# Kernel optimization log

Measured on AMD Instinct MI355X. Metric: run time of the kernel, lower is better.

The kernel has to match this reference:

```python
import jax, jax.numpy as jnp
import numpy as np

N = 20000   # nodes
E = 320000  # edges
L = 16      # text length per node
T = 64      # num_text_features
H = 128     # num_hidden_features
V = 32000   # vocab_size
NS = 2      # num_samples
C = 2       # num_classes
F = 8       # num_node_features


def setup_inputs() -> dict:
    key = jax.random.key(0)
    ks = jax.random.split(key, 20)
    def rn(k, shape, scale=0.05):
        return jax.random.normal(k, shape, jnp.float32) * scale
    return {
        "x": jax.random.normal(ks[0], (N, F), jnp.float32),
        "edge_index": jax.random.randint(ks[1], (2, E), 0, N),
        "xtext": jax.random.randint(ks[2], (N, L), 0, V),
        "image_features": jax.random.normal(ks[3], (N, H * NS), jnp.float32),
        "conv1_w": rn(ks[4], (F, H)), "conv1_b": jnp.zeros((H,), jnp.float32),
        "conv2_w": rn(ks[5], (H, H)), "conv2_b": jnp.zeros((H,), jnp.float32),
        "embed": rn(ks[6], (V, T), 1.0),
        "gru_wih": rn(ks[7], (3 * H, T)), "gru_whh": rn(ks[8], (3 * H, H)),
        "gru_bih": jnp.zeros((3 * H,), jnp.float32), "gru_bhh": jnp.zeros((3 * H,), jnp.float32),
        "lin_pos_w": rn(ks[9], (2 * H, H)), "lin_pos_b": jnp.zeros((H,), jnp.float32),
        "lin_text_w": rn(ks[10], (2 * H, H)), "lin_text_b": jnp.zeros((H,), jnp.float32),
        "lin_img_w": rn(ks[11], (2 * H * NS, H)), "lin_img_b": jnp.zeros((H,), jnp.float32),
        "row_w1": rn(ks[12], (3 * H, H)), "row_b1": jnp.zeros((H,), jnp.float32),
        "row_w2": rn(ks[13], (H, C)), "row_b2": jnp.zeros((C,), jnp.float32),
        "col_w1": rn(ks[14], (3 * H, H)), "col_b1": jnp.zeros((H,), jnp.float32),
        "col_w2": rn(ks[15], (H, C)), "col_b2": jnp.zeros((C,), jnp.float32),
    }


def gcn(x, w, b, src, dst, n):
    xw = x @ w  # [N, H]
    deg = jnp.zeros((n,), xw.dtype).at[dst].add(1.0) + 1.0
    dinv = jax.lax.rsqrt(deg)
    norm = dinv[src] * dinv[dst]  # [E]
    agg = jax.ops.segment_sum(xw[src] * norm[:, None], dst, num_segments=n)
    agg = agg + xw * (dinv * dinv)[:, None]  # self-loop term
    return agg + b


def gru_sum(x_seq, wih, whh, bih, bhh):
    # x_seq: [N, L, T]; torch GRU cell; return sum over time of outputs -> [N, H]
    h0 = jnp.zeros((x_seq.shape[0], whh.shape[1]), x_seq.dtype)
    def step(h, xt):
        gi = xt @ wih.T + bih
        gh = h @ whh.T + bhh
        ir, iz, inn = jnp.split(gi, 3, axis=-1)
        hr, hz, hn = jnp.split(gh, 3, axis=-1)
        r = jax.nn.sigmoid(ir + hr)
        z = jax.nn.sigmoid(iz + hz)
        nn_ = jnp.tanh(inn + r * hn)
        h2 = (1.0 - z) * nn_ + z * h
        return h2, h2
    _, ys = jax.lax.scan(step, h0, jnp.swapaxes(x_seq, 0, 1))  # ys: [L, N, H]
    return jnp.sum(ys, axis=0)


def reference(x, edge_index, xtext, image_features,
              conv1_w, conv1_b, conv2_w, conv2_b, embed,
              gru_wih, gru_whh, gru_bih, gru_bhh,
              lin_pos_w, lin_pos_b, lin_text_w, lin_text_b, lin_img_w, lin_img_b,
              row_w1, row_b1, row_w2, row_b2, col_w1, col_b1, col_w2, col_b2):
    src, dst = edge_index[0], edge_index[1]
    n = x.shape[0]
    h1 = jax.nn.relu(gcn(x, conv1_w, conv1_b, src, dst, n))
    pos = jax.nn.relu(gcn(h1, conv2_w, conv2_b, src, dst, n))
    txt = gru_sum(embed[xtext], gru_wih, gru_whh, gru_bih, gru_bhh)

    def edge_feat(feat, w, b):
        cat = jnp.concatenate([feat[src], feat[dst]], axis=1)
        return jax.nn.relu(cat @ w + b)

    ep = edge_feat(pos, lin_pos_w, lin_pos_b)
    et = edge_feat(txt, lin_text_w, lin_text_b)
    ei = edge_feat(image_features, lin_img_w, lin_img_b)
    e = jnp.concatenate([ep, et, ei], axis=1)  # [E, 3H]
    row_pred = jax.nn.log_softmax(jax.nn.relu(e @ row_w1 + row_b1) @ row_w2 + row_b2, axis=1)
    col_pred = jax.nn.log_softmax(jax.nn.relu(e @ col_w1 + col_b1) @ col_w2 + col_b2, axis=1)
    return (row_pred, col_pred)
```

## Files before the change

kernel.cpp:

```cpp
#include <hip/hip_runtime.h>
#include <hip/hip_bf16.h>

#define NN 20000
#define NE 320000
#define LL 16
#define TT 64
#define HH 128

typedef __attribute__((ext_vector_type(8))) short short8v;
typedef __attribute__((ext_vector_type(4))) float f32x4;
#define MFMA_BF16(a,b,c) __builtin_amdgcn_mfma_f32_16x16x32_bf16(a,b,c,0,0,0)

__device__ inline unsigned short f32_to_bf16(float v) {
  unsigned int b = __float_as_uint(v);
  b += 0x7fffu + ((b >> 16) & 1u);
  return (unsigned short)(b >> 16);
}
__device__ inline float bf16_to_f32(unsigned short u) {
  return __uint_as_float(((unsigned int)u) << 16);
}
__device__ inline float fast_sigmoid(float x) {
  return __builtin_amdgcn_rcpf(1.f + __expf(-x));
}
__device__ inline float fast_tanh(float x) {
  float e = __expf(2.f * x);
  return 1.f - 2.f * __builtin_amdgcn_rcpf(e + 1.f);
}
__device__ inline unsigned int cvt_pk_bf16(float lo, float hi) {
  unsigned int r;
  asm("v_cvt_pk_bf16_f32 %0, %1, %2" : "=v"(r) : "v"(lo), "v"(hi));
  return r;
}
__device__ inline unsigned int combine2(unsigned int us, unsigned int ud) {
  float sl = __uint_as_float(us << 16);
  float sh = __uint_as_float(us & 0xffff0000u);
  float dl = __uint_as_float(ud << 16);
  float dh = __uint_as_float(ud & 0xffff0000u);
  return cvt_pk_bf16(fmaxf(sl + dl, 0.f), fmaxf(sh + dh, 0.f));
}

__global__ void prep_k(
    const float* __restrict__ gwih, const float* __restrict__ gwhh,
    const float* __restrict__ rw1, const float* __restrict__ cw1,
    const float* __restrict__ conv2w,
    const float* __restrict__ lpw, const float* __restrict__ ltw, const float* __restrict__ liw,
    const float* __restrict__ lpb, const float* __restrict__ ltb, const float* __restrict__ lib,
    const float* __restrict__ gbih, const float* __restrict__ gbhh,
    unsigned short* __restrict__ wihB, unsigned short* __restrict__ whhB,
    unsigned short* __restrict__ rw1T, unsigned short* __restrict__ cw1T,
    unsigned short* __restrict__ conv2T,
    unsigned short* __restrict__ TposW, unsigned short* __restrict__ TtxtW,
    unsigned short* __restrict__ TimgW,
    float* __restrict__ bcomb, float* __restrict__ brz,
    float* __restrict__ binv, float* __restrict__ bhnv)
{
  int i = blockIdx.x * 256 + threadIdx.x;
  if (i < 24576) { wihB[i] = f32_to_bf16(gwih[i]); return; } i -= 24576;
  if (i < 49152) { whhB[i] = f32_to_bf16(gwhh[i]); return; } i -= 49152;
  if (i < 49152) { int c = i / 384, r = i - c * 384; rw1T[i] = f32_to_bf16(rw1[r * 128 + c]); return; } i -= 49152;
  if (i < 49152) { int c = i / 384, r = i - c * 384; cw1T[i] = f32_to_bf16(cw1[r * 128 + c]); return; } i -= 49152;
  if (i < 16384) { int c = i / 128, r = i - c * 128; conv2T[i] = f32_to_bf16(conv2w[r * 128 + c]); return; } i -= 16384;
  if (i < 32768) { int col = i / 128, k = i - col * 128;
    float v = (col < 128) ? lpw[k * 128 + col] : lpw[(128 + k) * 128 + (col - 128)];
    TposW[i] = f32_to_bf16(v); return; } i -= 32768;
  if (i < 32768) { int col = i / 128, k = i - col * 128;
    float v = (col < 128) ? ltw[k * 128 + col] : ltw[(128 + k) * 128 + (col - 128)];
    TtxtW[i] = f32_to_bf16(v); return; } i -= 32768;
  if (i < 65536) { int col = i / 256, k = i - col * 256;
    float v = (col < 128) ? liw[k * 128 + col] : liw[(256 + k) * 128 + (col - 128)];
    TimgW[i] = f32_to_bf16(v); return; } i -= 65536;
  if (i < 768) { int t = i >> 8, j = i & 255;
    const float* b = t == 0 ? lpb : t == 1 ? ltb : lib;
    bcomb[i] = (j < 128) ? 0.f : b[j - 128]; return; } i -= 768;
  if (i < 512) {
    if (i < 256) brz[i] = gbih[i] + gbhh[i];
    else if (i < 384) binv[i - 256] = gbih[i];
    else bhnv[i - 384] = gbhh[i - 128];
  }
}

__global__ void cvtf2_k(const float* __restrict__ in, unsigned int* __restrict__ out, int n2) {
  int i = blockIdx.x * 256 + threadIdx.x;
  if (i < n2) {
    float2 v = reinterpret_cast<const float2*>(in)[i];
    out[i] = cvt_pk_bf16(v.x, v.y);
  }
}

__global__ void fill_zero_k(float* __restrict__ p, int n) {
  int i = blockIdx.x * 256 + threadIdx.x;
  if (i < n) p[i] = 0.f;
}

__global__ void histo_k(const int* __restrict__ eidx, int* __restrict__ ideg) {
  int e = blockIdx.x * 256 + threadIdx.x;
  if (e < NE) atomicAdd(&ideg[eidx[NE + e]], 1);
}

__global__ void scan_k(const int* __restrict__ ideg, int* __restrict__ rowptr) {
  __shared__ int sh[256];
  __shared__ int carry;
  const int tid = threadIdx.x;
  if (tid == 0) carry = 0;
  __syncthreads();
  for (int base = 0; base < NN; base += 256) {
    int v = (base + tid < NN) ? ideg[base + tid] : 0;
    sh[tid] = v;
    __syncthreads();
#pragma unroll
    for (int off = 1; off < 256; off <<= 1) {
      int t = (tid >= off) ? sh[tid - off] : 0;
      __syncthreads();
      sh[tid] += t;
      __syncthreads();
    }
    if (base + tid < NN) rowptr[base + tid] = carry + sh[tid] - v;
    __syncthreads();
    if (tid == 255) carry += sh[255];
    __syncthreads();
  }
  if (tid == 0) rowptr[NN] = carry;
}

__global__ void dinv_csr_k(const int* __restrict__ rowptr, float* __restrict__ dinv) {
  int i = blockIdx.x * 256 + threadIdx.x;
  if (i < NN) dinv[i] = rsqrtf((float)(rowptr[i + 1] - rowptr[i]) + 1.f);
}

__global__ void scatter_k(const int* __restrict__ eidx, int* __restrict__ cursor,
                          int* __restrict__ esrc_s, int* __restrict__ edst_s,
                          int* __restrict__ eorig_s) {
  int e = blockIdx.x * 256 + threadIdx.x;
  if (e >= NE) return;
  int s = eidx[e], d = eidx[NE + e];
  int pos = atomicAdd(&cursor[d], 1);
  esrc_s[pos] = s;
  edst_s[pos] = d;
  eorig_s[pos] = e;
}

__global__ void xw1_k(const float* __restrict__ x, const float* __restrict__ w,
                      const float* __restrict__ dinv, unsigned int* __restrict__ xws) {
  int i = blockIdx.x * 256 + threadIdx.x;
  if (i >= NN * 64) return;
  int n = i >> 6, c2 = (i & 63) * 2;
  float a0 = 0.f, a1 = 0.f;
#pragma unroll
  for (int k = 0; k < 8; ++k) {
    float xv = x[n * 8 + k];
    a0 += xv * w[k * 128 + c2];
    a1 += xv * w[k * 128 + c2 + 1];
  }
  float dn = dinv[n];
  xws[i] = cvt_pk_bf16(a0 * dn, a1 * dn);
}

__global__ __launch_bounds__(256) void gcn_csr_k(
    const int* __restrict__ rowptr, const int* __restrict__ esrc_s,
    const unsigned int* __restrict__ xws, const float* __restrict__ dinv,
    const float* __restrict__ bias, unsigned int* __restrict__ outB)
{
  int node = blockIdx.x * 4 + (threadIdx.x >> 6);
  int lane = threadIdx.x & 63;
  if (node >= NN) return;
  float dd = dinv[node];
  int beg = rowptr[node], end = rowptr[node + 1];
  float a0 = 0.f, a1 = 0.f;
  int i = beg;
  for (; i + 1 < end; i += 2) {
    int s0 = esrc_s[i], s1 = esrc_s[i + 1];
    unsigned int u0 = xws[s0 * 64 + lane];
    unsigned int u1 = xws[s1 * 64 + lane];
    a0 += __uint_as_float(u0 << 16) + __uint_as_float(u1 << 16);
    a1 += __uint_as_float(u0 & 0xffff0000u) + __uint_as_float(u1 & 0xffff0000u);
  }
  if (i < end) {
    unsigned int u = xws[esrc_s[i] * 64 + lane];
    a0 += __uint_as_float(u << 16);
    a1 += __uint_as_float(u & 0xffff0000u);
  }
  unsigned int un = xws[node * 64 + lane];
  a0 += __uint_as_float(un << 16);
  a1 += __uint_as_float(un & 0xffff0000u);
  a0 = fmaxf(a0 * dd + bias[lane * 2], 0.f);
  a1 = fmaxf(a1 * dd + bias[lane * 2 + 1], 0.f);
  outB[node * 64 + lane] = cvt_pk_bf16(a0, a1);
}

template<int KDIM, int NCOLS, bool OUTBF16, bool ADDBIAS, bool SCALEROW>
__global__ __launch_bounds__(256) void gemm_mfma_k(
    const unsigned short* __restrict__ A, const unsigned short* __restrict__ WT,
    const float* __restrict__ bias, const float* __restrict__ rowscale,
    void* __restrict__ Cv, int M)
{
  const int tid = threadIdx.x;
  const int wid = tid >> 6, lane = tid & 63;
  const int l16 = lane & 15, lk = lane >> 4;
  const int bm = blockIdx.x * 128, bn = blockIdx.y * 128;
  const int wr = wid * 32;

  int row[2];
#pragma unroll
  for (int mf = 0; mf < 2; ++mf) {
    int r = bm + wr + mf * 16 + l16;
    row[mf] = r < M ? r : M - 1;
  }
  f32x4 acc[2][8];
#pragma unroll
  for (int mf = 0; mf < 2; ++mf)
#pragma unroll
    for (int nf = 0; nf < 8; ++nf) acc[mf][nf] = f32x4{0.f, 0.f, 0.f, 0.f};

#pragma unroll
  for (int kc = 0; kc < KDIM / 32; ++kc) {
    short8v a[2];
#pragma unroll
    for (int mf = 0; mf < 2; ++mf)
      a[mf] = *reinterpret_cast<const short8v*>(&A[(size_t)row[mf] * KDIM + kc * 32 + lk * 8]);
#pragma unroll
    for (int nf = 0; nf < 8; ++nf) {
      int col = bn + nf * 16 + l16;
      short8v b = *reinterpret_cast<const short8v*>(&WT[(size_t)col * KDIM + kc * 32 + lk * 8]);
      acc[0][nf] = MFMA_BF16(a[0], b, acc[0][nf]);
      acc[1][nf] = MFMA_BF16(a[1], b, acc[1][nf]);
    }
  }
#pragma unroll
  for (int mf = 0; mf < 2; ++mf)
#pragma unroll
    for (int nf = 0; nf < 8; ++nf) {
      int col = bn + nf * 16 + l16;
      float bb = ADDBIAS ? bias[col] : 0.f;
#pragma unroll
      for (int reg = 0; reg < 4; ++reg) {
        int r = bm + wr + mf * 16 + lk * 4 + reg;
        if (r < M) {
          float v = acc[mf][nf][reg] + bb;
          if (SCALEROW) v *= rowscale[r];
          if (OUTBF16) ((unsigned short*)Cv)[(size_t)r * NCOLS + col] = f32_to_bf16(v);
          else         ((float*)Cv)[(size_t)r * NCOLS + col] = v;
        }
      }
    }
}

__global__ __launch_bounds__(256, 2) void gru_fused_k(
    const int* __restrict__ xtext, const float* __restrict__ embed,
    const unsigned short* __restrict__ wihB, const unsigned short* __restrict__ whhB,
    const float* __restrict__ brz, const float* __restrict__ binv, const float* __restrict__ bhnv,
    unsigned short* __restrict__ txt)
{
  __shared__ unsigned char hs[2][32 * 256];
  __shared__ unsigned char xs[32 * 128];
  const int tid = threadIdx.x;
  const int n0 = blockIdx.x * 32;
  const int wid = tid >> 6, lane = tid & 63;
  const int l16 = lane & 15, lk = lane >> 4;

  for (int i = tid; i < 32 * 256 / 4; i += 256) ((unsigned int*)hs[0])[i] = 0u;

  short8v wR[2][2], wZ[2][2], wN[2][2];
  short8v uR[2][4], uZ[2][4], uN[2][4];
  float bRr[2], bZr[2], bIr[2], bHr[2];
#pragma unroll
  for (int cf = 0; cf < 2; ++cf) {
    int col = wid * 32 + cf * 16 + l16;
#pragma unroll
    for (int ks = 0; ks < 2; ++ks) {
      wR[cf][ks] = *reinterpret_cast<const short8v*>(&wihB[(col      ) * 64 + ks * 32 + lk * 8]);
      wZ[cf][ks] = *reinterpret_cast<const short8v*>(&wihB[(col + 128) * 64 + ks * 32 + lk * 8]);
      wN[cf][ks] = *reinterpret_cast<const short8v*>(&wihB[(col + 256) * 64 + ks * 32 + lk * 8]);
    }
#pragma unroll
    for (int ks = 0; ks < 4; ++ks) {
      uR[cf][ks] = *reinterpret_cast<const short8v*>(&whhB[(col      ) * 128 + ks * 32 + lk * 8]);
      uZ[cf][ks] = *reinterpret_cast<const short8v*>(&whhB[(col + 128) * 128 + ks * 32 + lk * 8]);
      uN[cf][ks] = *reinterpret_cast<const short8v*>(&whhB[(col + 256) * 128 + ks * 32 + lk * 8]);
    }
    bRr[cf] = brz[col]; bZr[cf] = brz[128 + col];
    bIr[cf] = binv[col]; bHr[cf] = bhnv[col];
  }

  f32x4 txtacc[2][2];
#pragma unroll
  for (int mf = 0; mf < 2; ++mf)
#pragma unroll
    for (int cf = 0; cf < 2; ++cf) txtacc[mf][cf] = f32x4{0.f, 0.f, 0.f, 0.f};

  int cur = 0;
  for (int t = 0; t < LL; ++t) {
    __syncthreads();
    {
      const int k4 = tid & 15, r0 = tid >> 4;
#pragma unroll
      for (int rep = 0; rep < 2; ++rep) {
        int row = r0 + rep * 16;
        int n = n0 + row; if (n >= NN) n = NN - 1;
        int tok = xtext[n * LL + t];
        float4 v = *reinterpret_cast<const float4*>(&embed[(size_t)tok * TT + k4 * 4]);
        ushort4 w;
        w.x = f32_to_bf16(v.x); w.y = f32_to_bf16(v.y);
        w.z = f32_to_bf16(v.z); w.w = f32_to_bf16(v.w);
        *reinterpret_cast<ushort4*>(&xs[row * 128 + ((k4 * 8) ^ ((row & 7) << 4))]) = w;
      }
    }
    __syncthreads();

#pragma unroll
    for (int mf = 0; mf < 2; ++mf) {
      const int arow = mf * 16 + l16;
      const int asw = (arow & 7) << 4;
      short8v ax[2], ah[4];
#pragma unroll
      for (int ks = 0; ks < 2; ++ks)
        ax[ks] = *reinterpret_cast<const short8v*>(&xs[arow * 128 + ((ks * 64 + lk * 16) ^ asw)]);
#pragma unroll
      for (int ks = 0; ks < 4; ++ks)
        ah[ks] = *reinterpret_cast<const short8v*>(&hs[cur][arow * 256 + ((ks * 64 + lk * 16) ^ asw)]);

      f32x4 aR[2], aZ[2], aI[2], aHn[2];
#pragma unroll
      for (int cf = 0; cf < 2; ++cf) {
        aR[cf] = f32x4{0.f, 0.f, 0.f, 0.f}; aZ[cf] = f32x4{0.f, 0.f, 0.f, 0.f};
        aI[cf] = f32x4{0.f, 0.f, 0.f, 0.f}; aHn[cf] = f32x4{0.f, 0.f, 0.f, 0.f};
#pragma unroll
        for (int ks = 0; ks < 2; ++ks) {
          aR[cf] = MFMA_BF16(ax[ks], wR[cf][ks], aR[cf]);
          aZ[cf] = MFMA_BF16(ax[ks], wZ[cf][ks], aZ[cf]);
          aI[cf] = MFMA_BF16(ax[ks], wN[cf][ks], aI[cf]);
        }
#pragma unroll
        for (int ks = 0; ks < 4; ++ks) {
          aR[cf]  = MFMA_BF16(ah[ks], uR[cf][ks], aR[cf]);
          aZ[cf]  = MFMA_BF16(ah[ks], uZ[cf][ks], aZ[cf]);
          aHn[cf] = MFMA_BF16(ah[ks], uN[cf][ks], aHn[cf]);
        }
      }

#pragma unroll
      for (int cf = 0; cf < 2; ++cf) {
        const int j = wid * 32 + cf * 16 + l16;
#pragma unroll
        for (int reg = 0; reg < 4; ++reg) {
          const int row = mf * 16 + lk * 4 + reg;
          const int byte = row * 256 + ((j * 2) ^ ((row & 7) << 4));
          float hold = bf16_to_f32(*reinterpret_cast<unsigned short*>(&hs[cur][byte]));
          float rg = fast_sigmoid(aR[cf][reg] + bRr[cf]);
          float zg = fast_sigmoid(aZ[cf][reg] + bZr[cf]);
          float ng = fast_tanh(aI[cf][reg] + bIr[cf] + rg * (aHn[cf][reg] + bHr[cf]));
          float h2 = (1.f - zg) * ng + zg * hold;
          txtacc[mf][cf][reg] += h2;
          *reinterpret_cast<unsigned short*>(&hs[cur ^ 1][byte]) = f32_to_bf16(h2);
        }
      }
    }
    cur ^= 1;
  }

#pragma unroll
  for (int mf = 0; mf < 2; ++mf)
#pragma unroll
    for (int cf = 0; cf < 2; ++cf) {
      const int j = wid * 32 + cf * 16 + l16;
#pragma unroll
      for (int reg = 0; reg < 4; ++reg) {
        const int row = mf * 16 + lk * 4 + reg;
        const int n = n0 + row;
        if (n < NN) txt[(size_t)n * HH + j] = f32_to_bf16(txtacc[mf][cf][reg]);
      }
    }
}

__global__ __launch_bounds__(256, 2) void edge_mfma_k(
    const int* __restrict__ esrc_s, const int* __restrict__ edst_s,
    const int* __restrict__ eorig_s,
    const unsigned short* __restrict__ Tall,
    const unsigned short* __restrict__ rw1T, const float* __restrict__ rb1,
    const float* __restrict__ rw2, const float* __restrict__ rb2,
    const unsigned short* __restrict__ cw1T, const float* __restrict__ cb1,
    const float* __restrict__ cw2, const float* __restrict__ cb2,
    float* __restrict__ out)
{
  const int tid = threadIdx.x;
  const int e0 = blockIdx.x * 128;
  const int wid = tid >> 6, lane = tid & 63;
  const int l16 = lane & 15, lk = lane >> 4;
  const int wr = wid * 32;
  const int lkoff = lk * 8;

  const int ea = e0 + wr + l16, eb = e0 + wr + 16 + l16;
  const size_t soff0 = (size_t)esrc_s[ea] * 256;
  const size_t soff1 = (size_t)esrc_s[eb] * 256;
  const size_t doff0 = (size_t)edst_s[ea] * 256 + 128;
  const size_t doff1 = (size_t)edst_s[eb] * 256 + 128;

  uint4 af[6][2][2];
  uint4 dr[2][2][2];
  f32x4 acc[2][8];
#pragma unroll
  for (int mf = 0; mf < 2; ++mf)
#pragma unroll
    for (int nf = 0; nf < 8; ++nf) acc[mf][nf] = f32x4{0.f, 0.f, 0.f, 0.f};

#define TB(c) (Tall + (size_t)((c) >> 1) * ((size_t)NN * 256) + ((c) & 1) * 64 + lkoff)
#define LSRC(c) { const unsigned short* tb = TB(c); \
  af[c][0][0] = *reinterpret_cast<const uint4*>(tb + soff0); \
  af[c][0][1] = *reinterpret_cast<const uint4*>(tb + soff0 + 32); \
  af[c][1][0] = *reinterpret_cast<const uint4*>(tb + soff1); \
  af[c][1][1] = *reinterpret_cast<const uint4*>(tb + soff1 + 32); }
#define LDST(c) { const unsigned short* tb = TB(c); \
  dr[(c) & 1][0][0] = *reinterpret_cast<const uint4*>(tb + doff0); \
  dr[(c) & 1][0][1] = *reinterpret_cast<const uint4*>(tb + doff0 + 32); \
  dr[(c) & 1][1][0] = *reinterpret_cast<const uint4*>(tb + doff1); \
  dr[(c) & 1][1][1] = *reinterpret_cast<const uint4*>(tb + doff1 + 32); }
#define COMB(c) { \
  _Pragma("unroll") for (int mf = 0; mf < 2; ++mf) \
  _Pragma("unroll") for (int ks = 0; ks < 2; ++ks) { \
    uint4 s = af[c][mf][ks], d = dr[(c) & 1][mf][ks]; \
    uint4 r; r.x = combine2(s.x, d.x); r.y = combine2(s.y, d.y); \
    r.z = combine2(s.z, d.z); r.w = combine2(s.w, d.w); \
    af[c][mf][ks] = r; } }
#define PROCH(c, W) { \
  _Pragma("unroll") for (int ks = 0; ks < 2; ++ks) { \
    short8v a0 = *reinterpret_cast<short8v*>(&af[c][0][ks]); \
    short8v a1 = *reinterpret_cast<short8v*>(&af[c][1][ks]); \
    int kglob = (c) * 64 + ks * 32 + lkoff; \
    _Pragma("unroll") for (int nf = 0; nf < 8; ++nf) { \
      int col = nf * 16 + l16; \
      short8v b = *reinterpret_cast<const short8v*>(&W[(size_t)col * 384 + kglob]); \
      acc[0][nf] = MFMA_BF16(a0, b, acc[0][nf]); \
      acc[1][nf] = MFMA_BF16(a1, b, acc[1][nf]); } } }
#define EPI(B1, W2, B2, H) { \
  _Pragma("unroll") for (int mf = 0; mf < 2; ++mf) \
  _Pragma("unroll") for (int reg = 0; reg < 4; ++reg) { \
    float p0 = 0.f, p1 = 0.f; \
    _Pragma("unroll") for (int nf = 0; nf < 8; ++nf) { \
      int col = nf * 16 + l16; \
      float hv = fmaxf(acc[mf][nf][reg] + B1[col], 0.f); \
      p0 += hv * W2[col * 2]; p1 += hv * W2[col * 2 + 1]; } \
    _Pragma("unroll") for (int m = 1; m < 16; m <<= 1) { \
      p0 += __shfl_xor(p0, m); p1 += __shfl_xor(p1, m); } \
    if (l16 == 0) { \
      int orig = eorig_s[e0 + wr + mf * 16 + lk * 4 + reg]; \
      float l0 = p0 + B2[0], l1 = p1 + B2[1]; \
      float mx = fmaxf(l0, l1); \
      float lse = mx + __logf(__expf(l0 - mx) + __expf(l1 - mx)); \
      float2 o2 = make_float2(l0 - lse, l1 - lse); \
      *reinterpret_cast<float2*>(&out[(size_t)(H) * 2 * NE + (size_t)orig * 2]) = o2; } } }

  LSRC(0) LSRC(1) LSRC(2) LSRC(3) LSRC(4) LSRC(5)
  LDST(0) LDST(1)
  COMB(0) PROCH(0, rw1T) LDST(2)
  COMB(1) PROCH(1, rw1T) LDST(3)
  COMB(2) PROCH(2, rw1T) LDST(4)
  COMB(3) PROCH(3, rw1T) LDST(5)
  COMB(4) PROCH(4, rw1T)
  COMB(5) PROCH(5, rw1T)
  EPI(rb1, rw2, rb2, 0)

#pragma unroll
  for (int mf = 0; mf < 2; ++mf)
#pragma unroll
    for (int nf = 0; nf < 8; ++nf) acc[mf][nf] = f32x4{0.f, 0.f, 0.f, 0.f};

  __builtin_amdgcn_s_setprio(1);
  PROCH(0, cw1T) PROCH(1, cw1T) PROCH(2, cw1T)
  PROCH(3, cw1T) PROCH(4, cw1T) PROCH(5, cw1T)
  __builtin_amdgcn_s_setprio(0);
  EPI(cb1, cw2, cb2, 1)

#undef TB
#undef LSRC
#undef LDST
#undef COMB
#undef PROCH
#undef EPI
}

extern "C" void kernel_launch(void* const* d_in, const int* in_sizes, int n_in,
                              void* d_out, int out_size, void* d_ws, size_t ws_size,
                              hipStream_t stream)
{
  const float* x       = (const float*)d_in[0];
  const int*   eidx    = (const int*)  d_in[1];
  const int*   xtext   = (const int*)  d_in[2];
  const float* imgf    = (const float*)d_in[3];
  const float* conv1_w = (const float*)d_in[4];
  const float* conv1_b = (const float*)d_in[5];
  const float* conv2_w = (const float*)d_in[6];
  const float* conv2_b = (const float*)d_in[7];
  const float* embed   = (const float*)d_in[8];
  const float* gwih    = (const float*)d_in[9];
  const float* gwhh    = (const float*)d_in[10];
  const float* gbih    = (const float*)d_in[11];
  const float* gbhh    = (const float*)d_in[12];
  const float* lpw     = (const float*)d_in[13];
  const float* lpb     = (const float*)d_in[14];
  const float* ltw     = (const float*)d_in[15];
  const float* ltb     = (const float*)d_in[16];
  const float* liw     = (const float*)d_in[17];
  const float* lib     = (const float*)d_in[18];
  const float* rw1     = (const float*)d_in[19];
  const float* rb1     = (const float*)d_in[20];
  const float* rw2     = (const float*)d_in[21];
  const float* rb2     = (const float*)d_in[22];
  const float* cw1     = (const float*)d_in[23];
  const float* cb1     = (const float*)d_in[24];
  const float* cw2     = (const float*)d_in[25];
  const float* cb2     = (const float*)d_in[26];
  float* out = (float*)d_out;

  char* w8 = (char*)d_ws;
  size_t off = 0;
  auto balloc = [&](size_t bytes) { void* p = w8 + off; off = (off + bytes + 255) & ~(size_t)255; return p; };
  float*          dinv   = (float*)balloc(NN * 4);
  int*            ideg   = (int*)balloc((NN + 1) * 4);
  int*            rowptr = (int*)balloc((NN + 1) * 4);
  int*            cursor = (int*)balloc((NN + 1) * 4);
  int*            esrc_s = (int*)balloc((size_t)NE * 4);
  int*            edst_s = (int*)balloc((size_t)NE * 4);
  int*            eorig_s= (int*)balloc((size_t)NE * 4);
  unsigned int*   xwsB   = (unsigned int*)balloc((size_t)NN * 64 * 4);
  unsigned int*   nodeB  = (unsigned int*)balloc((size_t)NN * 64 * 4);
  unsigned short* txtB   = (unsigned short*)balloc((size_t)NN * HH * 2);
  unsigned short* imgB   = (unsigned short*)balloc((size_t)NN * 256 * 2);
  unsigned short* Tall   = (unsigned short*)balloc((size_t)3 * NN * 256 * 2);
  unsigned short* wihB   = (unsigned short*)balloc(384 * 64 * 2);
  unsigned short* whhB   = (unsigned short*)balloc(384 * 128 * 2);
  unsigned short* rw1T   = (unsigned short*)balloc(384 * 128 * 2);
  unsigned short* cw1T   = (unsigned short*)balloc(384 * 128 * 2);
  unsigned short* conv2T = (unsigned short*)balloc(128 * 128 * 2);
  unsigned short* TposW  = (unsigned short*)balloc(256 * 128 * 2);
  unsigned short* TtxtW  = (unsigned short*)balloc(256 * 128 * 2);
  unsigned short* TimgW  = (unsigned short*)balloc(256 * 256 * 2);
  float*          bcomb  = (float*)balloc(768 * 4);
  float*          brz    = (float*)balloc(256 * 4);
  float*          binv   = (float*)balloc(128 * 4);
  float*          bhnv   = (float*)balloc(128 * 4);

  dim3 b256(256);
  auto cdiv = [](int a, int b) { return (a + b - 1) / b; };
  const int MB = cdiv(NN, 128);

  prep_k<<<cdiv(320768, 256), b256, 0, stream>>>(
      gwih, gwhh, rw1, cw1, conv2_w, lpw, ltw, liw, lpb, ltb, lib, gbih, gbhh,
      wihB, whhB, rw1T, cw1T, conv2T, TposW, TtxtW, TimgW, bcomb, brz, binv, bhnv);
  cvtf2_k<<<cdiv(NN * 128, 256), b256, 0, stream>>>(imgf, (unsigned int*)imgB, NN * 128);

  fill_zero_k<<<cdiv(NN + 1, 256), b256, 0, stream>>>((float*)ideg, NN + 1);
  histo_k<<<cdiv(NE, 256), b256, 0, stream>>>(eidx, ideg);
  scan_k<<<1, b256, 0, stream>>>(ideg, rowptr);
  dinv_csr_k<<<cdiv(NN, 256), b256, 0, stream>>>(rowptr, dinv);
  hipMemcpyAsync(cursor, rowptr, (NN + 1) * sizeof(int), hipMemcpyDeviceToDevice, stream);
  scatter_k<<<cdiv(NE, 256), b256, 0, stream>>>(eidx, cursor, esrc_s, edst_s, eorig_s);

  xw1_k<<<cdiv(NN * 64, 256), b256, 0, stream>>>(x, conv1_w, dinv, xwsB);
  gcn_csr_k<<<cdiv(NN, 4), b256, 0, stream>>>(rowptr, esrc_s, xwsB, dinv, conv1_b, nodeB);

  gemm_mfma_k<128, 128, true, false, true><<<dim3(MB, 1), b256, 0, stream>>>(
      (const unsigned short*)nodeB, conv2T, nullptr, dinv, xwsB, NN);
  gcn_csr_k<<<cdiv(NN, 4), b256, 0, stream>>>(rowptr, esrc_s, xwsB, dinv, conv2_b, nodeB);

  gru_fused_k<<<NN / 32, b256, 0, stream>>>(xtext, embed, wihB, whhB, brz, binv, bhnv, txtB);

  gemm_mfma_k<128, 256, true, true, false><<<dim3(MB, 2), b256, 0, stream>>>(
      (const unsigned short*)nodeB, TposW, bcomb, nullptr, Tall, NN);
  gemm_mfma_k<128, 256, true, true, false><<<dim3(MB, 2), b256, 0, stream>>>(
      txtB, TtxtW, bcomb + 256, nullptr, Tall + (size_t)NN * 256, NN);
  gemm_mfma_k<256, 256, true, true, false><<<dim3(MB, 2), b256, 0, stream>>>(
      imgB, TimgW, bcomb + 512, nullptr, Tall + (size_t)2 * NN * 256, NN);

  edge_mfma_k<<<NE / 128, b256, 0, stream>>>(esrc_s, edst_s, eorig_s, Tall,
                                             rw1T, rb1, rw2, rb2, cw1T, cb1, cw2, cb2, out);
}
```

Before: 795.6 us.

## Restructure edge kernel to 16 edges per wave with fused row/col heads

The edge MLP kernel now gives each wave 16 edges instead of 32 and computes the row and column hidden layers together in one pass over K. The A fragment is built once per K-slice and fed to both weight matrices, so the 6-chunk register cache of gathered features is no longer needed. Launch bounds rise to 4 blocks per SM and the grid doubles. The intent is lower register pressure and higher occupancy to hide gather latency. The cost is that each weight fragment load now serves half as many MFMAs, which increases weight traffic per edge.

Measured after the change: 998.7 us. +25.5%, slower.

```diff
diff --git a/kernel.cpp b/kernel.cpp
--- a/kernel.cpp
+++ b/kernel.cpp
@@ -371,7 +371,7 @@
     }
 }
 
-__global__ __launch_bounds__(256, 2) void edge_mfma_k(
+__global__ __launch_bounds__(256, 4) void edge_mfma_k(
     const int* __restrict__ esrc_s, const int* __restrict__ edst_s,
     const int* __restrict__ eorig_s,
     const unsigned short* __restrict__ Tall,
@@ -382,99 +382,89 @@
     float* __restrict__ out)
 {
   const int tid = threadIdx.x;
-  const int e0 = blockIdx.x * 128;
   const int wid = tid >> 6, lane = tid & 63;
   const int l16 = lane & 15, lk = lane >> 4;
-  const int wr = wid * 32;
+  const int e0 = blockIdx.x * 64 + wid * 16;
   const int lkoff = lk * 8;
 
-  const int ea = e0 + wr + l16, eb = e0 + wr + 16 + l16;
-  const size_t soff0 = (size_t)esrc_s[ea] * 256;
-  const size_t soff1 = (size_t)esrc_s[eb] * 256;
-  const size_t doff0 = (size_t)edst_s[ea] * 256 + 128;
-  const size_t doff1 = (size_t)edst_s[eb] * 256 + 128;
-
-  uint4 af[6][2][2];
-  uint4 dr[2][2][2];
-  f32x4 acc[2][8];
-#pragma unroll
-  for (int mf = 0; mf < 2; ++mf)
-#pragma unroll
-    for (int nf = 0; nf < 8; ++nf) acc[mf][nf] = f32x4{0.f, 0.f, 0.f, 0.f};
+  const size_t soff = (size_t)esrc_s[e0 + l16] * 256;
+  const size_t doff = (size_t)edst_s[e0 + l16] * 256 + 128;
+
+  f32x4 acc0[8], acc1[8];
+#pragma unroll
+  for (int nf = 0; nf < 8; ++nf) {
+    acc0[nf] = f32x4{0.f, 0.f, 0.f, 0.f};
+    acc1[nf] = f32x4{0.f, 0.f, 0.f, 0.f};
+  }
+
+  uint4 sr[2][2], dr[2][2];
 
 #define TB(c) (Tall + (size_t)((c) >> 1) * ((size_t)NN * 256) + ((c) & 1) * 64 + lkoff)
-#define LSRC(c) { const unsigned short* tb = TB(c); \
-  af[c][0][0] = *reinterpret_cast<const uint4*>(tb + soff0); \
-  af[c][0][1] = *reinterpret_cast<const uint4*>(tb + soff0 + 32); \
-  af[c][1][0] = *reinterpret_cast<const uint4*>(tb + soff1); \
-  af[c][1][1] = *reinterpret_cast<const uint4*>(tb + soff1 + 32); }
-#define LDST(c) { const unsigned short* tb = TB(c); \
-  dr[(c) & 1][0][0] = *reinterpret_cast<const uint4*>(tb + doff0); \
-  dr[(c) & 1][0][1] = *reinterpret_cast<const uint4*>(tb + doff0 + 32); \
-  dr[(c) & 1][1][0] = *reinterpret_cast<const uint4*>(tb + doff1); \
-  dr[(c) & 1][1][1] = *reinterpret_cast<const uint4*>(tb + doff1 + 32); }
-#define COMB(c) { \
-  _Pragma("unroll") for (int mf = 0; mf < 2; ++mf) \
+#define LD(c) { const unsigned short* tb = TB(c); \
+  sr[(c) & 1][0] = *reinterpret_cast<const uint4*>(tb + soff); \
+  sr[(c) & 1][1] = *reinterpret_cast<const uint4*>(tb + soff + 32); \
+  dr[(c) & 1][0] = *reinterpret_cast<const uint4*>(tb + doff); \
+  dr[(c) & 1][1] = *reinterpret_cast<const uint4*>(tb + doff + 32); }
+#define PROC(c) { \
   _Pragma("unroll") for (int ks = 0; ks < 2; ++ks) { \
-    uint4 s = af[c][mf][ks], d = dr[(c) & 1][mf][ks]; \
-    uint4 r; r.x = combine2(s.x, d.x); r.y = combine2(s.y, d.y); \
-    r.z = combine2(s.z, d.z); r.w = combine2(s.w, d.w); \
-    af[c][mf][ks] = r; } }
-#define PROCH(c, W) { \
-  _Pragma("unroll") for (int ks = 0; ks < 2; ++ks) { \
-    short8v a0 = *reinterpret_cast<short8v*>(&af[c][0][ks]); \
-    short8v a1 = *reinterpret_cast<short8v*>(&af[c][1][ks]); \
+    uint4 s = sr[(c) & 1][ks], d = dr[(c) & 1][ks]; \
+    unsigned int afr[4]; \
+    afr[0] = combine2(s.x, d.x); afr[1] = combine2(s.y, d.y); \
+    afr[2] = combine2(s.z, d.z); afr[3] = combine2(s.w, d.w); \
+    short8v a = *reinterpret_cast<short8v*>(afr); \
     int kglob = (c) * 64 + ks * 32 + lkoff; \
     _Pragma("unroll") for (int nf = 0; nf < 8; ++nf) { \
       int col = nf * 16 + l16; \
-      short8v b = *reinterpret_cast<const short8v*>(&W[(size_t)col * 384 + kglob]); \
-      acc[0][nf] = MFMA_BF16(a0, b, acc[0][nf]); \
-      acc[1][nf] = MFMA_BF16(a1, b, acc[1][nf]); } } }
-#define EPI(B1, W2, B2, H) { \
-  _Pragma("unroll") for (int mf = 0; mf < 2; ++mf) \
-  _Pragma("unroll") for (int reg = 0; reg < 4; ++reg) { \
-    float p0 = 0.f, p1 = 0.f; \
-    _Pragma("unroll") for (int nf = 0; nf < 8; ++nf) { \
-      int col = nf * 16 + l16; \
-      float hv = fmaxf(acc[mf][nf][reg] + B1[col], 0.f); \
-      p0 += hv * W2[col * 2]; p1 += hv * W2[col * 2 + 1]; } \
-    _Pragma("unroll") for (int m = 1; m < 16; m <<= 1) { \
-      p0 += __shfl_xor(p0, m); p1 += __shfl_xor(p1, m); } \
-    if (l16 == 0) { \
-      int orig = eorig_s[e0 + wr + mf * 16 + lk * 4 + reg]; \
-      float l0 = p0 + B2[0], l1 = p1 + B2[1]; \
-      float mx = fmaxf(l0, l1); \
-      float lse = mx + __logf(__expf(l0 - mx) + __expf(l1 - mx)); \
-      float2 o2 = make_float2(l0 - lse, l1 - lse); \
-      *reinterpret_cast<float2*>(&out[(size_t)(H) * 2 * NE + (size_t)orig * 2]) = o2; } } }
-
-  LSRC(0) LSRC(1) LSRC(2) LSRC(3) LSRC(4) LSRC(5)
-  LDST(0) LDST(1)
-  COMB(0) PROCH(0, rw1T) LDST(2)
-  COMB(1) PROCH(1, rw1T) LDST(3)
-  COMB(2) PROCH(2, rw1T) LDST(4)
-  COMB(3) PROCH(3, rw1T) LDST(5)
-  COMB(4) PROCH(4, rw1T)
-  COMB(5) PROCH(5, rw1T)
-  EPI(rb1, rw2, rb2, 0)
-
-#pragma unroll
-  for (int mf = 0; mf < 2; ++mf)
-#pragma unroll
-    for (int nf = 0; nf < 8; ++nf) acc[mf][nf] = f32x4{0.f, 0.f, 0.f, 0.f};
-
-  __builtin_amdgcn_s_setprio(1);
-  PROCH(0, cw1T) PROCH(1, cw1T) PROCH(2, cw1T)
-  PROCH(3, cw1T) PROCH(4, cw1T) PROCH(5, cw1T)
-  __builtin_amdgcn_s_setprio(0);
-  EPI(cb1, cw2, cb2, 1)
-
+      short8v br = *reinterpret_cast<const short8v*>(&rw1T[(size_t)col * 384 + kglob]); \
+      acc0[nf] = MFMA_BF16(a, br, acc0[nf]); \
+      short8v bc = *reinterpret_cast<const short8v*>(&cw1T[(size_t)col * 384 + kglob]); \
+      acc1[nf] = MFMA_BF16(a, bc, acc1[nf]); \
+    } \
+  } }
+
+  LD(0)
+  LD(1)
+  PROC(0) LD(2)
+  PROC(1) LD(3)
+  PROC(2) LD(4)
+  PROC(3) LD(5)
+  PROC(4)
+  PROC(5)
 #undef TB
-#undef LSRC
-#undef LDST
-#undef COMB
-#undef PROCH
-#undef EPI
+#undef LD
+#undef PROC
+
+#pragma unroll
+  for (int h = 0; h < 2; ++h) {
+    const f32x4* ac = h ? acc1 : acc0;
+    const float* b1 = h ? cb1 : rb1;
+    const float* w2 = h ? cw2 : rw2;
+    const float* b2 = h ? cb2 : rb2;
+#pragma unroll
+    for (int reg = 0; reg < 4; ++reg) {
+      float p0 = 0.f, p1 = 0.f;
+#pragma unroll
+      for (int nf = 0; nf < 8; ++nf) {
+        int col = nf * 16 + l16;
+        float hv = fmaxf(ac[nf][reg] + b1[col], 0.f);
+        p0 += hv * w2[col * 2];
+        p1 += hv * w2[col * 2 + 1];
+      }
+#pragma unroll
+      for (int m = 1; m < 16; m <<= 1) {
+        p0 += __shfl_xor(p0, m);
+        p1 += __shfl_xor(p1, m);
+      }
+      if (l16 == 0) {
+        int orig = eorig_s[e0 + lk * 4 + reg];
+        float l0 = p0 + b2[0], l1 = p1 + b2[1];
+        float mx = fmaxf(l0, l1);
+        float lse = mx + __logf(__expf(l0 - mx) + __expf(l1 - mx));
+        float2 o2 = make_float2(l0 - lse, l1 - lse);
+        *reinterpret_cast<float2*>(&out[(size_t)h * 2 * NE + (size_t)orig * 2]) = o2;
+      }
+    }
+  }
 }
 
 extern "C" void kernel_launch(void* const* d_in, const int* in_sizes, int n_in,
@@ -570,6 +560,6 @@
   gemm_mfma_k<256, 256, true, true, false><<<dim3(MB, 2), b256, 0, stream>>>(
       imgB, TimgW, bcomb + 512, nullptr, Tall + (size_t)2 * NN * 256, NN);
 
-  edge_mfma_k<<<NE / 128, b256, 0, stream>>>(esrc_s, edst_s, eorig_s, Tall,
-                                             rw1T, rb1, rw2, rb2, cw1T, cb1, cw2, cb2, out);
-}
+  edge_mfma_k<<<NE / 64, b256, 0, stream>>>(esrc_s, edst_s, eorig_s, Tall,
+                                            rw1T, rb1, rw2, rb2, cw1T, cb1, cw2, cb2, out);
+}
```

## Stage edge MLP weights in LDS and swizzle blocks across XCDs

Applied to the files above, without the earlier changes.

The edge kernel now copies the 384x128 bf16 first-layer weight matrix (row head, then column head) into 96 KB of shared memory before each head and reads B fragments from LDS instead of global memory. It also remaps block indices so that consecutive edge tiles land on the same XCD, for better L2 locality of node feature gathers. Launch bounds drop to one block per SM and the setprio hint is removed. The cost is extra barriers, restaging the weights for the second head, and lower occupancy from the large LDS footprint, which could hurt latency hiding for the gathers.

Result: faster. 711.5 us (-10.6%).

```diff
diff --git a/kernel.cpp b/kernel.cpp
--- a/kernel.cpp
+++ b/kernel.cpp
@@ -371,7 +371,7 @@
     }
 }
 
-__global__ __launch_bounds__(256, 2) void edge_mfma_k(
+__global__ __launch_bounds__(256, 1) void edge_mfma_k(
     const int* __restrict__ esrc_s, const int* __restrict__ edst_s,
     const int* __restrict__ eorig_s,
     const unsigned short* __restrict__ Tall,
@@ -381,8 +381,12 @@
     const float* __restrict__ cw2, const float* __restrict__ cb2,
     float* __restrict__ out)
 {
+  __shared__ __align__(16) unsigned char wlds[98304];
   const int tid = threadIdx.x;
-  const int e0 = blockIdx.x * 128;
+  const int bid = blockIdx.x;
+  const int xcd = bid & 7, bi = bid >> 3;
+  const int swz = (xcd < 4 ? xcd * 313 : 4 * 313 + (xcd - 4) * 312) + bi;
+  const int e0 = swz * 128;
   const int wid = tid >> 6, lane = tid & 63;
   const int l16 = lane & 15, lk = lane >> 4;
   const int wr = wid * 32;
@@ -420,14 +424,22 @@
     uint4 r; r.x = combine2(s.x, d.x); r.y = combine2(s.y, d.y); \
     r.z = combine2(s.z, d.z); r.w = combine2(s.w, d.w); \
     af[c][mf][ks] = r; } }
-#define PROCH(c, W) { \
+#define STAGEW(W) { \
+  _Pragma("unroll") for (int s2 = 0; s2 < 3; ++s2) { \
+    int s = wid * 3 + s2; \
+    int kg = (s >> 1) * 64 + (s & 1) * 32; \
+    _Pragma("unroll") for (int i = 0; i < 8; ++i) { \
+      int col = i * 16 + (lane >> 2); \
+      uint4 t = *reinterpret_cast<const uint4*>(&W[(size_t)col * 384 + kg + (lane & 3) * 8]); \
+      *reinterpret_cast<uint4*>(&wlds[s * 8192 + i * 1024 + lane * 16]) = t; \
+    } } }
+#define PROCHL(c) { \
   _Pragma("unroll") for (int ks = 0; ks < 2; ++ks) { \
     short8v a0 = *reinterpret_cast<short8v*>(&af[c][0][ks]); \
     short8v a1 = *reinterpret_cast<short8v*>(&af[c][1][ks]); \
-    int kglob = (c) * 64 + ks * 32 + lkoff; \
+    const unsigned char* wb = &wlds[((c) * 2 + ks) * 8192 + lk * 16]; \
     _Pragma("unroll") for (int nf = 0; nf < 8; ++nf) { \
-      int col = nf * 16 + l16; \
-      short8v b = *reinterpret_cast<const short8v*>(&W[(size_t)col * 384 + kglob]); \
+      short8v b = *reinterpret_cast<const short8v*>(wb + (nf * 16 + l16) * 64); \
       acc[0][nf] = MFMA_BF16(a0, b, acc[0][nf]); \
       acc[1][nf] = MFMA_BF16(a1, b, acc[1][nf]); } } }
 #define EPI(B1, W2, B2, H) { \
@@ -450,30 +462,34 @@
 
   LSRC(0) LSRC(1) LSRC(2) LSRC(3) LSRC(4) LSRC(5)
   LDST(0) LDST(1)
-  COMB(0) PROCH(0, rw1T) LDST(2)
-  COMB(1) PROCH(1, rw1T) LDST(3)
-  COMB(2) PROCH(2, rw1T) LDST(4)
-  COMB(3) PROCH(3, rw1T) LDST(5)
-  COMB(4) PROCH(4, rw1T)
-  COMB(5) PROCH(5, rw1T)
+  STAGEW(rw1T)
+  __syncthreads();
+
+  COMB(0) PROCHL(0) LDST(2)
+  COMB(1) PROCHL(1) LDST(3)
+  COMB(2) PROCHL(2) LDST(4)
+  COMB(3) PROCHL(3) LDST(5)
+  COMB(4) PROCHL(4)
+  COMB(5) PROCHL(5)
   EPI(rb1, rw2, rb2, 0)
 
+  __syncthreads();
+  STAGEW(cw1T)
+  __syncthreads();
+
 #pragma unroll
   for (int mf = 0; mf < 2; ++mf)
 #pragma unroll
     for (int nf = 0; nf < 8; ++nf) acc[mf][nf] = f32x4{0.f, 0.f, 0.f, 0.f};
-
-  __builtin_amdgcn_s_setprio(1);
-  PROCH(0, cw1T) PROCH(1, cw1T) PROCH(2, cw1T)
-  PROCH(3, cw1T) PROCH(4, cw1T) PROCH(5, cw1T)
-  __builtin_amdgcn_s_setprio(0);
+  PROCHL(0) PROCHL(1) PROCHL(2) PROCHL(3) PROCHL(4) PROCHL(5)
   EPI(cb1, cw2, cb2, 1)
 
 #undef TB
 #undef LSRC
 #undef LDST
 #undef COMB
-#undef PROCH
+#undef STAGEW
+#undef PROCHL
 #undef EPI
 }
 
```
